# Kernel tuning notes

Hardware: AMD Instinct MI355X
Metric: run time of the kernel (lower is better)

## Reference

```python
import jax, jax.numpy as jnp
import numpy as np

B = 128
IN = 256
NLVL = 6
KLVL = 3
CH = 4
C = 4 * CH * CH          # 64 channels per node
OU = 8                   # out_filter_siz_u
OV = 8                   # out_filter_siz_v
NK = 2 ** KLVL           # 8 leaf nodes per axis
W_SCALE = 1.0 / 16.0     # ~1/sqrt(2*2*C) so 7 stacked relu-convs stay numerically sane


def setup_inputs() -> dict:
    key = jax.random.key(0)
    ks = jax.random.split(key, 2 * NLVL + 4)
    fx = IN // 2 ** NLVL  # 4: input patch filter size
    inp = {}
    inp["in_data"] = jax.random.normal(ks[0], (B, IN, IN, 1), jnp.float32)
    inp["in_filter"] = jax.random.normal(ks[1], (fx, fx, 1, C), jnp.float32) * W_SCALE
    inp["in_bias"] = jnp.zeros((C,), jnp.float32)
    i = 2
    for lvl in range(1, NLVL + 1):
        n = 2 ** min(lvl, KLVL)  # node grid: grows to 2^klvl then stays
        inp[f"f{lvl}"] = jax.random.normal(ks[i], (n, n, 2, 2, C, C), jnp.float32) * W_SCALE
        inp[f"b{lvl}"] = jnp.zeros((n, n, C), jnp.float32)
        i += 1
    inp["Wd"] = jax.random.normal(ks[i], (NK, NK, 2, C, OU * OV), jnp.float32) * W_SCALE
    return inp


def _node_conv(x, w, b):
    # x: [Nu,Nv,B,H,W,C]; w: [Nu,Nv,2,2,C,C]; 2x2 stride-2 VALID conv per node
    Nu, Nv, Bn, H, W, Cc = x.shape
    xr = x.reshape(Nu, Nv, Bn, H // 2, 2, W // 2, 2, Cc)
    y = jnp.einsum('uvbhxwyc,uvxyco->uvbhwo', xr, w)
    return jax.nn.relu(y + b[:, :, None, None, None, :])


def _forward(in_data, in_filter, in_bias, fs, bs, Wd):
    Bn = in_data.shape[0]
    fx, fy = in_filter.shape[0], in_filter.shape[1]
    # input interp conv: stride == kernel -> non-overlapping patch GEMM
    xr = in_data[..., 0].reshape(Bn, in_data.shape[1] // fx, fx, in_data.shape[2] // fy, fy)
    x = jax.nn.relu(jnp.einsum('bxpyq,pqc->bxyc', xr, in_filter[:, :, 0, :]) + in_bias)
    x = x[None, None]  # [1,1,B,2^nlvl,2^nlvl,C] node grid
    for lvl in range(1, NLVL + 1):
        if lvl <= KLVL:
            # children (itu,itv) read parent (itu//2, itv//2)
            x = jnp.repeat(jnp.repeat(x, 2, axis=0), 2, axis=1)
        x = _node_conv(x, fs[lvl - 1], bs[lvl - 1])
    feats = x[:, :, :, 0, 0, :]  # [NK,NK,B,C]; spatial is 1x1 at level nlvl
    out = jnp.einsum('uvbc,uvrck->uvbrk', feats, Wd)  # r in {real, imag}
    out = out.reshape(NK, NK, Bn, 2, OU, OV)
    out = jnp.transpose(out, (2, 0, 4, 1, 5, 3))  # [B,itu,ou,itv,ov,2]
    return out.reshape(Bn, NK * OU, NK * OV, 2)


def reference(in_data, in_filter, in_bias, f1, b1, f2, b2, f3, b3, f4, b4, f5, b5, f6, b6, Wd):
    fs = (f1, f2, f3, f4, f5, f6)
    bs = (b1, b2, b3, b4, b5, b6)
    return _forward(in_data, in_filter, in_bias, fs, bs, Wd)
```

## Files before the change

kernel.cpp:

```cpp
#include <hip/hip_runtime.h>
#include <hip/hip_bf16.h>
#include <cstdint>
#include <cstddef>


typedef __attribute__((ext_vector_type(8))) short short8;
typedef __attribute__((ext_vector_type(4))) float f32x4;
typedef unsigned short ushort_t;

static __device__ __forceinline__ float b2f(const __hip_bfloat16 x) {
    return __bfloat162float(x);
}
static __device__ __forceinline__ ushort_t f2bf(float x) {
    __hip_bfloat16 h = __float2bfloat16(x);
    ushort_t u;
    __builtin_memcpy(&u, &h, 2);
    return u;
}
static __device__ __forceinline__ void gl_lds16(const void* g, void* l) {
    __builtin_amdgcn_global_load_lds(
        (const __attribute__((address_space(1))) void*)g,
        (__attribute__((address_space(3))) void*)l, 16, 0, 0);
}

__global__ void k_detect(const uint32_t* __restrict__ in, int* __restrict__ flag) {
    const int t = threadIdx.x;
    const float v = __uint_as_float(in[t]);
    const bool plaus = (v == 0.0f) || (fabsf(v) > 1e-8f && fabsf(v) < 1e4f);
    const unsigned long long m = __ballot(plaus);
    if (t == 0) *flag = (__popcll(m) >= 48) ? 0 : 1;
}

__global__ __launch_bounds__(256) void k_prepw(
    const void* f1, const void* f2, const void* f3,
    const void* f4, const void* f5, const void* f6,
    ushort_t* __restrict__ wbuf, const int* __restrict__ flag)
{
    const int isbf = *flag;
    const int gid = blockIdx.x * 256 + threadIdx.x;
    const void* fsrc; int base;
    if      (gid <   8192) { fsrc = f1; base = 0;      }
    else if (gid <  40960) { fsrc = f2; base = 8192;   }
    else if (gid < 172032) { fsrc = f3; base = 40960;  }
    else if (gid < 303104) { fsrc = f4; base = 172032; }
    else if (gid < 434176) { fsrc = f5; base = 303104; }
    else if (gid < 565248) { fsrc = f6; base = 434176; }
    else return;
    const int local = gid - base;
    const int lane = local & 63;
    const int slot = (local >> 6) & 7;
    const int sitetap = local >> 9;
    const int ks = slot >> 2, nh = slot & 3, q = lane >> 4;
    const int n = (lane & 15) + nh * 16;
    const int kbase = ks * 32 + q * 8;
    ushort_t pk[8];
    if (isbf) {
        const ushort_t* s = (const ushort_t*)fsrc + (size_t)sitetap * 4096;
        #pragma unroll
        for (int j = 0; j < 8; j++) pk[j] = s[(kbase + j) * 64 + n];
    } else {
        const float* s = (const float*)fsrc + (size_t)sitetap * 4096;
        #pragma unroll
        for (int j = 0; j < 8; j++) pk[j] = f2bf(s[(kbase + j) * 64 + n]);
    }
    *(uint4*)&wbuf[(size_t)gid * 8] = *(uint4*)pk;
}

__global__ __launch_bounds__(256) void k_prepb(
    const void* b1, const void* b2, const void* b3,
    const void* b4, const void* b5, const void* b6,
    float* __restrict__ bbuf, const int* __restrict__ flag)
{
    const int isbf = *flag;
    const int gid = blockIdx.x * 256 + threadIdx.x;
    const void* src; int base;
    if      (gid <   256) { src = b1; base = 0;     }
    else if (gid <  1280) { src = b2; base = 256;   }
    else if (gid <  5376) { src = b3; base = 1280;  }
    else if (gid <  9472) { src = b4; base = 5376;  }
    else if (gid < 13568) { src = b5; base = 9472;  }
    else if (gid < 17664) { src = b6; base = 13568; }
    else return;
    const int local = gid - base;
    bbuf[gid] = isbf ? b2f(((const __hip_bfloat16*)src)[local])
                     : ((const float*)src)[local];
}

__global__ __launch_bounds__(256) void k_stage0(
    const void* __restrict__ in_data, const void* __restrict__ filt,
    const void* __restrict__ bias, __hip_bfloat16* __restrict__ x0,
    const int* __restrict__ flag, int b_off)
{
    const int isbf = *flag;
    const int blk = blockIdx.x;
    const int X  = blk & 63;
    const int bl = blk >> 6;
    const int bg = bl + b_off;

    __shared__ float sIn[4][256];
    __shared__ float sF[16][64];
    __shared__ float sB[64];

    const int t = threadIdx.x;
    const size_t srow = ((size_t)bg * 256 + (size_t)X * 4) * 256;

    if (isbf) {
        const __hip_bfloat16* src = (const __hip_bfloat16*)in_data + srow;
        #pragma unroll
        for (int i = 0; i < 4; i++) {
            int flat = i * 256 + t;
            int p = flat >> 8, col = flat & 255;
            sIn[p][col] = b2f(src[(size_t)p * 256 + col]);
        }
        const __hip_bfloat16* fsrc = (const __hip_bfloat16*)filt;
        #pragma unroll
        for (int i = 0; i < 4; i++) {
            int flat = i * 256 + t;
            sF[flat >> 6][flat & 63] = b2f(fsrc[flat]);
        }
        if (t < 64) sB[t] = b2f(((const __hip_bfloat16*)bias)[t]);
    } else {
        const float* src = (const float*)in_data + srow;
        #pragma unroll
        for (int i = 0; i < 4; i++) {
            int flat = i * 256 + t;
            int p = flat >> 8, col = flat & 255;
            sIn[p][col] = src[(size_t)p * 256 + col];
        }
        const float* fsrc = (const float*)filt;
        #pragma unroll
        for (int i = 0; i < 4; i++) {
            int flat = i * 256 + t;
            sF[flat >> 6][flat & 63] = fsrc[flat];
        }
        if (t < 64) sB[t] = ((const float*)bias)[t];
    }
    __syncthreads();

    __hip_bfloat16* dst = x0 + ((size_t)bl * 64 + X) * 64 * 64;
    #pragma unroll
    for (int i = 0; i < 16; i++) {
        int flat = i * 256 + t;
        int c = flat & 63, Y = flat >> 6;
        float acc = sB[c];
        #pragma unroll
        for (int p = 0; p < 4; p++) {
            #pragma unroll
            for (int q = 0; q < 4; q++) {
                acc = fmaf(sIn[p][Y * 4 + q], sF[p * 4 + q][c], acc);
            }
        }
        dst[(size_t)Y * 64 + c] = __float2bfloat16(fmaxf(acc, 0.f));
    }
}

__global__ __launch_bounds__(256) void k_level4(
    const __hip_bfloat16* __restrict__ xin,
    const ushort_t* __restrict__ wbuf,
    const float* __restrict__ bbuf,
    __hip_bfloat16* __restrict__ xout,
    int Nv_out, int HW, int Bc, int mtiles)
{
    __shared__ ushort_t smem[20480];
    __shared__ float sBias[4][64];
    ushort_t* sA = smem;
    ushort_t* sB = smem + 4096;

    int idx = blockIdx.x;
    const int mt = idx % mtiles; idx /= mtiles;
    const int w  = idx % HW; idx /= HW;
    const int h  = idx % HW; idx /= HW;
    const int Nv_in = Nv_out >> 1;
    const int vp = idx % Nv_in;
    const int up = idx / Nv_in;

    const int t = threadIdx.x;
    const int wave = t >> 6, lane = t & 63;
    const int lm = lane & 15, lq = lane >> 4;

    {
        const int ct = t >> 6, o = t & 63;
        const int so_t = (2 * up + (ct >> 1)) * Nv_out + (2 * vp + (ct & 1));
        sBias[ct][o] = bbuf[so_t * 64 + o];
    }

    const int so = (2 * up + (wave >> 1)) * Nv_out + (2 * vp + (wave & 1));
    const int H_in = HW * 2;
    const size_t bstride = (size_t)H_in * H_in * 64;
    const size_t siteb = (size_t)(up * Nv_in + vp) * Bc * bstride;
    const ushort_t* wsite = wbuf + (size_t)so * 4 * 4096;

    const f32x4 zero = {0.f, 0.f, 0.f, 0.f};
    f32x4 acc[4][4];
    #pragma unroll
    for (int i = 0; i < 4; i++)
        #pragma unroll
        for (int j = 0; j < 4; j++) acc[i][j] = zero;

    for (int tap = 0; tap < 4; tap++) {
        const int hi = 2 * h + (tap >> 1), wi = 2 * w + (tap & 1);
        const size_t tapoff = siteb + ((size_t)hi * H_in + wi) * 64;
        #pragma unroll
        for (int s2 = 0; s2 < 2; s2++) {
            const int s = wave * 2 + s2;
            const int ks = s >> 2, mh = s & 3;
            int b = mt * 64 + lm + mh * 16;
            if (b >= Bc) b = Bc - 1;
            gl_lds16(xin + tapoff + (size_t)b * bstride + ks * 32 + lq * 8,
                     &sA[s * 512]);
        }
        const ushort_t* wt = wsite + (size_t)tap * 4096;
        #pragma unroll
        for (int s = 0; s < 8; s++) {
            gl_lds16(wt + s * 512 + lane * 8, &sB[wave * 4096 + s * 512]);
        }
        __syncthreads();

        #pragma unroll
        for (int ks = 0; ks < 2; ks++) {
            short8 bf0 = *(const short8*)&sB[wave * 4096 + (ks * 4 + 0) * 512 + lane * 8];
            short8 bf1 = *(const short8*)&sB[wave * 4096 + (ks * 4 + 1) * 512 + lane * 8];
            short8 bf2 = *(const short8*)&sB[wave * 4096 + (ks * 4 + 2) * 512 + lane * 8];
            short8 bf3 = *(const short8*)&sB[wave * 4096 + (ks * 4 + 3) * 512 + lane * 8];
            #pragma unroll
            for (int fm = 0; fm < 4; fm++) {
                short8 a = *(const short8*)&sA[(ks * 4 + fm) * 512 + lane * 8];
                acc[fm][0] = __builtin_amdgcn_mfma_f32_16x16x32_bf16(a, bf0, acc[fm][0], 0, 0, 0);
                acc[fm][1] = __builtin_amdgcn_mfma_f32_16x16x32_bf16(a, bf1, acc[fm][1], 0, 0, 0);
                acc[fm][2] = __builtin_amdgcn_mfma_f32_16x16x32_bf16(a, bf2, acc[fm][2], 0, 0, 0);
                acc[fm][3] = __builtin_amdgcn_mfma_f32_16x16x32_bf16(a, bf3, acc[fm][3], 0, 0, 0);
            }
        }
        __syncthreads();
    }

    float bv[4];
    #pragma unroll
    for (int fn = 0; fn < 4; fn++) bv[fn] = sBias[wave][fn * 16 + lm];
    ushort_t* so_buf = smem + wave * 4352;
    #pragma unroll
    for (int fm = 0; fm < 4; fm++) {
        #pragma unroll
        for (int fn = 0; fn < 4; fn++) {
            #pragma unroll
            for (int r = 0; r < 4; r++) {
                const int row = fm * 16 + lq * 4 + r;
                so_buf[row * 68 + fn * 16 + lm] =
                    f2bf(fmaxf(acc[fm][fn][r] + bv[fn], 0.f));
            }
        }
    }
    __syncthreads();

    const size_t ostride = (size_t)HW * HW * 64;
    const size_t obase = (size_t)so * Bc * ostride + ((size_t)h * HW + w) * 64;
    #pragma unroll
    for (int i = 0; i < 8; i++) {
        const int task = i * 64 + lane;
        const int oct = task & 7, row = task >> 3;
        const int b = mt * 64 + row;
        if (b < Bc) {
            *(uint4*)(xout + obase + (size_t)b * ostride + oct * 8) =
                *(const uint4*)&so_buf[row * 68 + oct * 8];
        }
    }
}

__global__ __launch_bounds__(256) void k_level1(
    const __hip_bfloat16* __restrict__ xin,
    const ushort_t* __restrict__ wbuf,
    const float* __restrict__ bbuf,
    __hip_bfloat16* __restrict__ xout,
    int Nv, int HW, int Bc, int mtiles)
{
    __shared__ ushort_t smem[12288];
    __shared__ float sBias[64];
    ushort_t* sA = smem;
    ushort_t* sB = smem + 8192;

    int idx = blockIdx.x;
    const int mt = idx % mtiles; idx /= mtiles;
    const int w  = idx % HW; idx /= HW;
    const int h  = idx % HW; idx /= HW;
    const int site = idx;

    const int t = threadIdx.x;
    const int wave = t >> 6, lane = t & 63;
    const int lm = lane & 15, lq = lane >> 4;

    if (t < 64) sBias[t] = bbuf[site * 64 + t];

    const int H_in = HW * 2;
    const size_t bstride = (size_t)H_in * H_in * 64;
    const size_t siteb = (size_t)site * Bc * bstride;
    const ushort_t* wsite = wbuf + (size_t)site * 4 * 4096;

    const f32x4 zero = {0.f, 0.f, 0.f, 0.f};
    f32x4 acc[2][4];
    #pragma unroll
    for (int i = 0; i < 2; i++)
        #pragma unroll
        for (int j = 0; j < 4; j++) acc[i][j] = zero;

    for (int tap = 0; tap < 4; tap++) {
        const int hi = 2 * h + (tap >> 1), wi = 2 * w + (tap & 1);
        const size_t tapoff = siteb + ((size_t)hi * H_in + wi) * 64;
        #pragma unroll
        for (int s2 = 0; s2 < 4; s2++) {
            const int s = wave * 4 + s2;
            const int ks = s >> 3, mh = s & 7;
            int b = mt * 128 + lm + mh * 16;
            if (b >= Bc) b = Bc - 1;
            gl_lds16(xin + tapoff + (size_t)b * bstride + ks * 32 + lq * 8,
                     &sA[s * 512]);
        }
        const ushort_t* wt = wsite + (size_t)tap * 4096;
        #pragma unroll
        for (int s2 = 0; s2 < 2; s2++) {
            const int s = wave * 2 + s2;
            gl_lds16(wt + s * 512 + lane * 8, &sB[s * 512]);
        }
        __syncthreads();

        #pragma unroll
        for (int ks = 0; ks < 2; ks++) {
            short8 bf0 = *(const short8*)&sB[(ks * 4 + 0) * 512 + lane * 8];
            short8 bf1 = *(const short8*)&sB[(ks * 4 + 1) * 512 + lane * 8];
            short8 bf2 = *(const short8*)&sB[(ks * 4 + 2) * 512 + lane * 8];
            short8 bf3 = *(const short8*)&sB[(ks * 4 + 3) * 512 + lane * 8];
            #pragma unroll
            for (int fml = 0; fml < 2; fml++) {
                short8 a = *(const short8*)&sA[(ks * 8 + wave * 2 + fml) * 512 + lane * 8];
                acc[fml][0] = __builtin_amdgcn_mfma_f32_16x16x32_bf16(a, bf0, acc[fml][0], 0, 0, 0);
                acc[fml][1] = __builtin_amdgcn_mfma_f32_16x16x32_bf16(a, bf1, acc[fml][1], 0, 0, 0);
                acc[fml][2] = __builtin_amdgcn_mfma_f32_16x16x32_bf16(a, bf2, acc[fml][2], 0, 0, 0);
                acc[fml][3] = __builtin_amdgcn_mfma_f32_16x16x32_bf16(a, bf3, acc[fml][3], 0, 0, 0);
            }
        }
        __syncthreads();
    }

    float bv[4];
    #pragma unroll
    for (int fn = 0; fn < 4; fn++) bv[fn] = sBias[fn * 16 + lm];
    ushort_t* so_buf = smem;
    #pragma unroll
    for (int fml = 0; fml < 2; fml++) {
        #pragma unroll
        for (int fn = 0; fn < 4; fn++) {
            #pragma unroll
            for (int r = 0; r < 4; r++) {
                const int row = wave * 32 + fml * 16 + lq * 4 + r;
                so_buf[row * 68 + fn * 16 + lm] =
                    f2bf(fmaxf(acc[fml][fn][r] + bv[fn], 0.f));
            }
        }
    }
    __syncthreads();

    const size_t ostride = (size_t)HW * HW * 64;
    const size_t obase = (size_t)site * Bc * ostride + ((size_t)h * HW + w) * 64;
    #pragma unroll
    for (int i = 0; i < 4; i++) {
        const int task = i * 256 + t;
        const int oct = task & 7, row = task >> 3;
        const int b = mt * 128 + row;
        if (b < Bc) {
            *(uint4*)(xout + obase + (size_t)b * ostride + oct * 8) =
                *(const uint4*)&so_buf[row * 68 + oct * 8];
        }
    }
}

__global__ __launch_bounds__(256) void k_final(
    const __hip_bfloat16* __restrict__ feats, const void* __restrict__ Wd,
    void* __restrict__ out, const int* __restrict__ flag, int Bc, int b_off)
{
    const int isbf = *flag;
    const int uv = blockIdx.x;
    const int u = uv >> 3, v = uv & 7;
    const int b0 = blockIdx.y * 32;

    __shared__ float sF[32][64];
    __shared__ float sW[2][64][64];

    const int t = threadIdx.x;

    const __hip_bfloat16* fsrc = feats + (size_t)uv * Bc * 64;
    #pragma unroll
    for (int i = 0; i < 8; i++) {
        int flat = i * 256 + t;
        int row = flat >> 6;
        int brow = b0 + row;
        if (brow >= Bc) brow = Bc - 1;
        sF[row][flat & 63] = b2f(fsrc[(size_t)brow * 64 + (flat & 63)]);
    }
    const size_t woff = (size_t)uv * 2 * 64 * 64;
    if (isbf) {
        const __hip_bfloat16* wsrc = (const __hip_bfloat16*)Wd + woff;
        #pragma unroll
        for (int i = 0; i < 32; i++) {
            int flat = i * 256 + t;
            ((float*)sW)[flat] = b2f(wsrc[flat]);
        }
    } else {
        const float* wsrc = (const float*)Wd + woff;
        #pragma unroll
        for (int i = 0; i < 32; i++) {
            int flat = i * 256 + t;
            ((float*)sW)[flat] = wsrc[flat];
        }
    }
    __syncthreads();

    #pragma unroll
    for (int i = 0; i < 16; i++) {
        int flat = i * 256 + t;
        int k = flat & 63;
        int r = (flat >> 6) & 1;
        int b = flat >> 7;
        if (b0 + b >= Bc) continue;
        float acc = 0.f;
        #pragma unroll 8
        for (int c = 0; c < 64; c++) acc = fmaf(sF[b][c], sW[r][c][k], acc);
        const int bg = b_off + b0 + b;
        const int ou = k >> 3, ov = k & 7;
        const size_t oidx = (((size_t)bg * 64 + (u * 8 + ou)) * 64 + (v * 8 + ov)) * 2 + r;
        if (isbf) ((__hip_bfloat16*)out)[oidx] = __float2bfloat16(acc);
        else      ((float*)out)[oidx] = acc;
    }
}

extern "C" void kernel_launch(void* const* d_in, const int* in_sizes, int n_in,
                              void* d_out, int out_size, void* d_ws, size_t ws_size,
                              hipStream_t stream)
{
    (void)in_sizes; (void)n_in; (void)out_size;

    const void* in_data = d_in[0];
    const void* filt    = d_in[1];
    const void* bias0   = d_in[2];
    const void* fl[7];
    const void* bl[7];
    for (int l = 1; l <= 6; l++) {
        fl[l] = d_in[1 + 2 * l];
        bl[l] = d_in[2 + 2 * l];
    }
    const void* Wd = d_in[15];

    const int Bfull = 128;
    const size_t perB = (size_t)64 * 64 * 64;

    const size_t wbufBytes = 4521984ull * 2;
    const size_t bbufBytes = 17664ull * 4;
    const size_t headBytes = 256 + wbufBytes + bbufBytes;

    const size_t avail = ws_size > headBytes ? ws_size - headBytes : 0;
    int Bc = 0;
    for (int c = 128; c >= 1; c >>= 1) {
        if ((size_t)2 * c * perB * sizeof(__hip_bfloat16) <= avail) { Bc = c; break; }
    }
    if (Bc == 0) return;

    int* flag = (int*)d_ws;
    ushort_t* wbuf = (ushort_t*)((char*)d_ws + 256);
    float* bbuf = (float*)((char*)d_ws + 256 + wbufBytes);
    __hip_bfloat16* bufA = (__hip_bfloat16*)((char*)d_ws + headBytes);
    __hip_bfloat16* bufB = bufA + (size_t)Bc * perB;

    static const size_t w_off[7] = {0, 0, 65536, 327680, 1376256, 2424832, 3473408};
    static const int    b_off_tab[7] = {0, 0, 256, 1280, 5376, 9472, 13568};

    k_detect<<<dim3(1), 64, 0, stream>>>((const uint32_t*)in_data, flag);
    k_prepw<<<dim3(2208), 256, 0, stream>>>(fl[1], fl[2], fl[3], fl[4], fl[5], fl[6], wbuf, flag);
    k_prepb<<<dim3(69), 256, 0, stream>>>(bl[1], bl[2], bl[3], bl[4], bl[5], bl[6], bbuf, flag);

    const int mt4 = (Bc + 63) / 64;
    const int mt1 = (Bc + 127) / 128;

    for (int b_off = 0; b_off < Bfull; b_off += Bc) {
        k_stage0<<<dim3(Bc * 64), 256, 0, stream>>>(in_data, filt, bias0, bufA, flag, b_off);

        __hip_bfloat16* cur = bufA;
        __hip_bfloat16* nxt = bufB;
        for (int lvl = 1; lvl <= 6; lvl++) {
            const int Nu = 1 << (lvl < 3 ? lvl : 3);
            const int H  = 64 >> lvl;
            if (lvl <= 3) {
                const int Nv_in = Nu >> 1;
                dim3 grid(Nv_in * Nv_in * H * H * mt4);
                k_level4<<<grid, 256, 0, stream>>>(cur, wbuf + w_off[lvl],
                    bbuf + b_off_tab[lvl], nxt, Nu, H, Bc, mt4);
            } else {
                dim3 grid(Nu * Nu * H * H * mt1);
                k_level1<<<grid, 256, 0, stream>>>(cur, wbuf + w_off[lvl],
                    bbuf + b_off_tab[lvl], nxt, Nu, H, Bc, mt1);
            }
            __hip_bfloat16* tmp = cur; cur = nxt; nxt = tmp;
        }

        dim3 fgrid(64, (Bc >= 32) ? (Bc / 32) : 1);
        k_final<<<fgrid, 256, 0, stream>>>(cur, Wd, d_out, flag, Bc, b_off);
    }
}
```

Baseline: 292.9 us.

## Fuse level-6 conv with final projection via MFMA; vectorize stage0 input conv

Replaces the separate level-6 conv and scalar final projection with one k_tail kernel per site. It computes the level-6 2x2 conv with bf16 MFMA, keeps the result in LDS, and applies the Wd projection with MFMA, using a pre-packed bf16 Wd buffer added to k_prepw. Stage0 now uses float4 loads and a 4x4 register-tiled FMA loop with packed bf16 stores. This removes one launch and an intermediate round trip, but k_tail runs only 64 blocks and rounds Wd and features to bf16.

```diff
diff --git a/kernel.cpp b/kernel.cpp
--- a/kernel.cpp
+++ b/kernel.cpp
@@ -33,19 +33,44 @@
 
 __global__ __launch_bounds__(256) void k_prepw(
     const void* f1, const void* f2, const void* f3,
-    const void* f4, const void* f5, const void* f6,
-    ushort_t* __restrict__ wbuf, const int* __restrict__ flag)
+    const void* f4, const void* f5, const void* f6, const void* wdsrc,
+    ushort_t* __restrict__ wbuf, ushort_t* __restrict__ wdbuf,
+    const int* __restrict__ flag)
 {
     const int isbf = *flag;
     const int gid = blockIdx.x * 256 + threadIdx.x;
+    if (gid >= 630784) return;
+    if (gid >= 565248) {
+        const int local = gid - 565248;
+        const int lane = local & 63;
+        const int slot = (local >> 6) & 15;
+        const int site = local >> 10;
+        const int ks2 = slot >> 3, nh = slot & 7, q = lane >> 4;
+        const int n = nh * 16 + (lane & 15);
+        const int r = n >> 6, kk = n & 63;
+        const int cbase = ks2 * 32 + q * 8;
+        ushort_t pk[8];
+        if (isbf) {
+            const ushort_t* s = (const ushort_t*)wdsrc;
+            #pragma unroll
+            for (int j = 0; j < 8; j++)
+                pk[j] = s[(((size_t)(site * 2 + r) * 64 + cbase + j) * 64) + kk];
+        } else {
+            const float* s = (const float*)wdsrc;
+            #pragma unroll
+            for (int j = 0; j < 8; j++)
+                pk[j] = f2bf(s[(((size_t)(site * 2 + r) * 64 + cbase + j) * 64) + kk]);
+        }
+        *(uint4*)&wdbuf[(size_t)local * 8] = *(uint4*)pk;
+        return;
+    }
     const void* fsrc; int base;
     if      (gid <   8192) { fsrc = f1; base = 0;      }
     else if (gid <  40960) { fsrc = f2; base = 8192;   }
     else if (gid < 172032) { fsrc = f3; base = 40960;  }
     else if (gid < 303104) { fsrc = f4; base = 172032; }
     else if (gid < 434176) { fsrc = f5; base = 303104; }
-    else if (gid < 565248) { fsrc = f6; base = 434176; }
-    else return;
+    else                   { fsrc = f6; base = 434176; }
     const int local = gid - base;
     const int lane = local & 63;
     const int slot = (local >> 6) & 7;
@@ -121,12 +146,8 @@
         if (t < 64) sB[t] = b2f(((const __hip_bfloat16*)bias)[t]);
     } else {
         const float* src = (const float*)in_data + srow;
-        #pragma unroll
-        for (int i = 0; i < 4; i++) {
-            int flat = i * 256 + t;
-            int p = flat >> 8, col = flat & 255;
-            sIn[p][col] = src[(size_t)p * 256 + col];
-        }
+        const int p = t >> 6, c4 = (t & 63) * 4;
+        *(float4*)&sIn[p][c4] = *(const float4*)(src + (size_t)p * 256 + c4);
         const float* fsrc = (const float*)filt;
         #pragma unroll
         for (int i = 0; i < 4; i++) {
@@ -137,20 +158,50 @@
     }
     __syncthreads();
 
-    __hip_bfloat16* dst = x0 + ((size_t)bl * 64 + X) * 64 * 64;
-    #pragma unroll
-    for (int i = 0; i < 16; i++) {
-        int flat = i * 256 + t;
-        int c = flat & 63, Y = flat >> 6;
-        float acc = sB[c];
-        #pragma unroll
-        for (int p = 0; p < 4; p++) {
+    const int ty = t >> 4;
+    const int tc = t & 15;
+
+    float acc[4][4];
+    {
+        const float4 bv = *(const float4*)&sB[tc * 4];
+        #pragma unroll
+        for (int yi = 0; yi < 4; yi++) {
+            acc[yi][0] = bv.x; acc[yi][1] = bv.y;
+            acc[yi][2] = bv.z; acc[yi][3] = bv.w;
+        }
+    }
+
+    #pragma unroll
+    for (int p = 0; p < 4; p++) {
+        float4 rin[4], rf[4];
+        #pragma unroll
+        for (int yi = 0; yi < 4; yi++)
+            rin[yi] = *(const float4*)&sIn[p][ty * 16 + yi * 4];
+        #pragma unroll
+        for (int q = 0; q < 4; q++)
+            rf[q] = *(const float4*)&sF[p * 4 + q][tc * 4];
+        #pragma unroll
+        for (int yi = 0; yi < 4; yi++) {
             #pragma unroll
             for (int q = 0; q < 4; q++) {
-                acc = fmaf(sIn[p][Y * 4 + q], sF[p * 4 + q][c], acc);
-            }
-        }
-        dst[(size_t)Y * 64 + c] = __float2bfloat16(fmaxf(acc, 0.f));
+                const float a = ((const float*)&rin[yi])[q];
+                acc[yi][0] = fmaf(a, rf[q].x, acc[yi][0]);
+                acc[yi][1] = fmaf(a, rf[q].y, acc[yi][1]);
+                acc[yi][2] = fmaf(a, rf[q].z, acc[yi][2]);
+                acc[yi][3] = fmaf(a, rf[q].w, acc[yi][3]);
+            }
+        }
+    }
+
+    ushort_t* dst = (ushort_t*)(x0 + ((size_t)bl * 64 + X) * 64 * 64);
+    #pragma unroll
+    for (int yi = 0; yi < 4; yi++) {
+        uint2 pk;
+        pk.x = (uint32_t)f2bf(fmaxf(acc[yi][0], 0.f))
+             | ((uint32_t)f2bf(fmaxf(acc[yi][1], 0.f)) << 16);
+        pk.y = (uint32_t)f2bf(fmaxf(acc[yi][2], 0.f))
+             | ((uint32_t)f2bf(fmaxf(acc[yi][3], 0.f)) << 16);
+        *(uint2*)(dst + (size_t)(ty * 4 + yi) * 64 + tc * 4) = pk;
     }
 }
 
@@ -372,62 +423,133 @@
     }
 }
 
-__global__ __launch_bounds__(256) void k_final(
-    const __hip_bfloat16* __restrict__ feats, const void* __restrict__ Wd,
-    void* __restrict__ out, const int* __restrict__ flag, int Bc, int b_off)
+__global__ __launch_bounds__(256) void k_tail(
+    const __hip_bfloat16* __restrict__ xin,
+    const ushort_t* __restrict__ w6,
+    const float* __restrict__ b6,
+    const ushort_t* __restrict__ wd,
+    void* __restrict__ out,
+    const int* __restrict__ flag, int Bc, int b_off)
 {
     const int isbf = *flag;
-    const int uv = blockIdx.x;
-    const int u = uv >> 3, v = uv & 7;
-    const int b0 = blockIdx.y * 32;
-
-    __shared__ float sF[32][64];
-    __shared__ float sW[2][64][64];
+    const int site = blockIdx.x;
+    const int u = site >> 3, v = site & 7;
+
+    __shared__ ushort_t sA[16 * 512];
+    __shared__ ushort_t sB1[8 * 512];
+    __shared__ ushort_t sMid[128 * 72];
+    __shared__ float sBias[64];
 
     const int t = threadIdx.x;
-
-    const __hip_bfloat16* fsrc = feats + (size_t)uv * Bc * 64;
-    #pragma unroll
-    for (int i = 0; i < 8; i++) {
-        int flat = i * 256 + t;
-        int row = flat >> 6;
-        int brow = b0 + row;
-        if (brow >= Bc) brow = Bc - 1;
-        sF[row][flat & 63] = b2f(fsrc[(size_t)brow * 64 + (flat & 63)]);
-    }
-    const size_t woff = (size_t)uv * 2 * 64 * 64;
-    if (isbf) {
-        const __hip_bfloat16* wsrc = (const __hip_bfloat16*)Wd + woff;
-        #pragma unroll
-        for (int i = 0; i < 32; i++) {
-            int flat = i * 256 + t;
-            ((float*)sW)[flat] = b2f(wsrc[flat]);
-        }
-    } else {
-        const float* wsrc = (const float*)Wd + woff;
-        #pragma unroll
-        for (int i = 0; i < 32; i++) {
-            int flat = i * 256 + t;
-            ((float*)sW)[flat] = wsrc[flat];
-        }
+    const int wave = t >> 6, lane = t & 63;
+    const int lm = lane & 15, lq = lane >> 4;
+
+    if (t < 64) sBias[t] = b6[site * 64 + t];
+
+    const f32x4 zero = {0.f, 0.f, 0.f, 0.f};
+    f32x4 acc1[2][4];
+    #pragma unroll
+    for (int i = 0; i < 2; i++)
+        #pragma unroll
+        for (int j = 0; j < 4; j++) acc1[i][j] = zero;
+
+    const size_t abase = (size_t)site * Bc * 256;
+
+    for (int chunk = 0; chunk < 4; chunk++) {
+        #pragma unroll
+        for (int s2 = 0; s2 < 4; s2++) {
+            const int s = wave * 4 + s2;
+            const int ks = s >> 3, mh = s & 7;
+            int b = mh * 16 + lm;
+            if (b >= Bc) b = Bc - 1;
+            gl_lds16(xin + abase + (size_t)b * 256 + chunk * 64 + ks * 32 + lq * 8,
+                     &sA[s * 512]);
+        }
+        const ushort_t* wt = w6 + (size_t)(site * 4 + chunk) * 4096;
+        #pragma unroll
+        for (int s2 = 0; s2 < 2; s2++) {
+            const int s = wave * 2 + s2;
+            gl_lds16(wt + s * 512 + lane * 8, &sB1[s * 512]);
+        }
+        __syncthreads();
+
+        #pragma unroll
+        for (int ks = 0; ks < 2; ks++) {
+            short8 bf0 = *(const short8*)&sB1[(ks * 4 + 0) * 512 + lane * 8];
+            short8 bf1 = *(const short8*)&sB1[(ks * 4 + 1) * 512 + lane * 8];
+            short8 bf2 = *(const short8*)&sB1[(ks * 4 + 2) * 512 + lane * 8];
+            short8 bf3 = *(const short8*)&sB1[(ks * 4 + 3) * 512 + lane * 8];
+            #pragma unroll
+            for (int fml = 0; fml < 2; fml++) {
+                short8 a = *(const short8*)&sA[(ks * 8 + wave * 2 + fml) * 512 + lane * 8];
+                acc1[fml][0] = __builtin_amdgcn_mfma_f32_16x16x32_bf16(a, bf0, acc1[fml][0], 0, 0, 0);
+                acc1[fml][1] = __builtin_amdgcn_mfma_f32_16x16x32_bf16(a, bf1, acc1[fml][1], 0, 0, 0);
+                acc1[fml][2] = __builtin_amdgcn_mfma_f32_16x16x32_bf16(a, bf2, acc1[fml][2], 0, 0, 0);
+                acc1[fml][3] = __builtin_amdgcn_mfma_f32_16x16x32_bf16(a, bf3, acc1[fml][3], 0, 0, 0);
+            }
+        }
+        __syncthreads();
+    }
+
+    float bv[4];
+    #pragma unroll
+    for (int fn = 0; fn < 4; fn++) bv[fn] = sBias[fn * 16 + lm];
+    #pragma unroll
+    for (int fml = 0; fml < 2; fml++) {
+        #pragma unroll
+        for (int fn = 0; fn < 4; fn++) {
+            #pragma unroll
+            for (int r = 0; r < 4; r++) {
+                const int row = wave * 32 + fml * 16 + lq * 4 + r;
+                sMid[row * 72 + fn * 16 + lm] =
+                    f2bf(fmaxf(acc1[fml][fn][r] + bv[fn], 0.f));
+            }
+        }
+    }
+    #pragma unroll
+    for (int s2 = 0; s2 < 4; s2++) {
+        const int s = wave * 4 + s2;
+        gl_lds16(wd + ((size_t)(site * 16 + s) * 64 + lane) * 8, &sA[s * 512]);
     }
     __syncthreads();
 
-    #pragma unroll
-    for (int i = 0; i < 16; i++) {
-        int flat = i * 256 + t;
-        int k = flat & 63;
-        int r = (flat >> 6) & 1;
-        int b = flat >> 7;
-        if (b0 + b >= Bc) continue;
-        float acc = 0.f;
-        #pragma unroll 8
-        for (int c = 0; c < 64; c++) acc = fmaf(sF[b][c], sW[r][c][k], acc);
-        const int bg = b_off + b0 + b;
-        const int ou = k >> 3, ov = k & 7;
-        const size_t oidx = (((size_t)bg * 64 + (u * 8 + ou)) * 64 + (v * 8 + ov)) * 2 + r;
-        if (isbf) ((__hip_bfloat16*)out)[oidx] = __float2bfloat16(acc);
-        else      ((float*)out)[oidx] = acc;
+    f32x4 acc2[2][8];
+    #pragma unroll
+    for (int i = 0; i < 2; i++)
+        #pragma unroll
+        for (int j = 0; j < 8; j++) acc2[i][j] = zero;
+
+    #pragma unroll
+    for (int ks2 = 0; ks2 < 2; ks2++) {
+        short8 a20 = *(const short8*)&sMid[((wave * 2 + 0) * 16 + lm) * 72 + ks2 * 32 + lq * 8];
+        short8 a21 = *(const short8*)&sMid[((wave * 2 + 1) * 16 + lm) * 72 + ks2 * 32 + lq * 8];
+        #pragma unroll
+        for (int nh = 0; nh < 8; nh++) {
+            short8 bv2 = *(const short8*)&sA[(ks2 * 8 + nh) * 512 + lane * 8];
+            acc2[0][nh] = __builtin_amdgcn_mfma_f32_16x16x32_bf16(a20, bv2, acc2[0][nh], 0, 0, 0);
+            acc2[1][nh] = __builtin_amdgcn_mfma_f32_16x16x32_bf16(a21, bv2, acc2[1][nh], 0, 0, 0);
+        }
+    }
+
+    #pragma unroll
+    for (int fml = 0; fml < 2; fml++) {
+        #pragma unroll
+        for (int nh = 0; nh < 8; nh++) {
+            const int n = nh * 16 + lm;
+            const int r = n >> 6, ou = (n >> 3) & 7, ov = n & 7;
+            const size_t obase =
+                (((size_t)0 * 64 + (u * 8 + ou)) * 64 + (v * 8 + ov)) * 2 + r;
+            #pragma unroll
+            for (int reg = 0; reg < 4; reg++) {
+                const int brow = wave * 32 + fml * 16 + lq * 4 + reg;
+                if (brow < Bc) {
+                    const size_t oidx = obase + (size_t)(b_off + brow) * 8192;
+                    if (isbf) ((__hip_bfloat16*)out)[oidx] =
+                        __float2bfloat16(acc2[fml][nh][reg]);
+                    else ((float*)out)[oidx] = acc2[fml][nh][reg];
+                }
+            }
+        }
     }
 }
 
@@ -451,9 +573,10 @@
     const int Bfull = 128;
     const size_t perB = (size_t)64 * 64 * 64;
 
-    const size_t wbufBytes = 4521984ull * 2;
-    const size_t bbufBytes = 17664ull * 4;
-    const size_t headBytes = 256 + wbufBytes + bbufBytes;
+    const size_t wbufBytes  = 565248ull * 16;
+    const size_t wdbufBytes = 65536ull * 16;
+    const size_t bbufBytes  = 17664ull * 4;
+    const size_t headBytes  = 256 + wbufBytes + wdbufBytes + bbufBytes;
 
     const size_t avail = ws_size > headBytes ? ws_size - headBytes : 0;
     int Bc = 0;
@@ -463,8 +586,9 @@
     if (Bc == 0) return;
 
     int* flag = (int*)d_ws;
-    ushort_t* wbuf = (ushort_t*)((char*)d_ws + 256);
-    float* bbuf = (float*)((char*)d_ws + 256 + wbufBytes);
+    ushort_t* wbuf  = (ushort_t*)((char*)d_ws + 256);
+    ushort_t* wdbuf = (ushort_t*)((char*)d_ws + 256 + wbufBytes);
+    float* bbuf = (float*)((char*)d_ws + 256 + wbufBytes + wdbufBytes);
     __hip_bfloat16* bufA = (__hip_bfloat16*)((char*)d_ws + headBytes);
     __hip_bfloat16* bufB = bufA + (size_t)Bc * perB;
 
@@ -472,7 +596,8 @@
     static const int    b_off_tab[7] = {0, 0, 256, 1280, 5376, 9472, 13568};
 
     k_detect<<<dim3(1), 64, 0, stream>>>((const uint32_t*)in_data, flag);
-    k_prepw<<<dim3(2208), 256, 0, stream>>>(fl[1], fl[2], fl[3], fl[4], fl[5], fl[6], wbuf, flag);
+    k_prepw<<<dim3(2464), 256, 0, stream>>>(fl[1], fl[2], fl[3], fl[4], fl[5], fl[6],
+                                            Wd, wbuf, wdbuf, flag);
     k_prepb<<<dim3(69), 256, 0, stream>>>(bl[1], bl[2], bl[3], bl[4], bl[5], bl[6], bbuf, flag);
 
     const int mt4 = (Bc + 63) / 64;
@@ -483,7 +608,7 @@
 
         __hip_bfloat16* cur = bufA;
         __hip_bfloat16* nxt = bufB;
-        for (int lvl = 1; lvl <= 6; lvl++) {
+        for (int lvl = 1; lvl <= 5; lvl++) {
             const int Nu = 1 << (lvl < 3 ? lvl : 3);
             const int H  = 64 >> lvl;
             if (lvl <= 3) {
@@ -499,7 +624,7 @@
             __hip_bfloat16* tmp = cur; cur = nxt; nxt = tmp;
         }
 
-        dim3 fgrid(64, (Bc >= 32) ? (Bc / 32) : 1);
-        k_final<<<fgrid, 256, 0, stream>>>(cur, Wd, d_out, flag, Bc, b_off);
-    }
-}
+        k_tail<<<dim3(64), 256, 0, stream>>>(cur, wbuf + w_off[6],
+            bbuf + b_off_tab[6], wdbuf, d_out, flag, Bc, b_off);
+    }
+}
```

New measurement: 266.6 us. 1.1x faster.
